# Optimization experiments

Measured on AMD Instinct MI355X. Metric: run time of the kernel, lower is better.

Reference implementation:

```python
import jax, jax.numpy as jnp
import numpy as np

N, E = 50000, 800000
IN_DIM, HID, OUT = 128, 64, 64
NEG_SLOPE = 0.2  # PyG GATConv default leaky_relu slope


def glorot(key, shape):
    fan_in, fan_out = shape[0], shape[-1]
    lim = jnp.sqrt(6.0 / (fan_in + fan_out))
    return jax.random.uniform(key, shape, minval=-lim, maxval=lim, dtype=jnp.float32)


def setup_inputs() -> dict:
    key = jax.random.key(0)
    ks = jax.random.split(key, 10)
    x = jax.random.normal(ks[0], (N, IN_DIM), dtype=jnp.float32)
    edge_index = jax.random.randint(ks[1], (2, E), 0, N, dtype=jnp.int64)
    # GATConv layer 1: heads=2, concat=False
    W1 = glorot(ks[2], (IN_DIM, 2 * HID))
    att_src1 = glorot(ks[3], (1, 2, HID))[0]   # [2, HID]
    att_dst1 = glorot(ks[4], (1, 2, HID))[0]
    b1 = jnp.zeros((HID,), jnp.float32)
    # GATConv layer 2: heads=1, concat=False
    W2 = glorot(ks[5], (HID, OUT))
    att_src2 = glorot(ks[6], (1, 1, OUT))[0]   # [1, OUT]
    att_dst2 = glorot(ks[7], (1, 1, OUT))[0]
    b2 = jnp.zeros((OUT,), jnp.float32)
    return {"x": x, "edge_index": edge_index, "W1": W1, "att_src1": att_src1,
            "att_dst1": att_dst1, "b1": b1, "W2": W2, "att_src2": att_src2,
            "att_dst2": att_dst2, "b2": b2}


def gat_conv(x, src, dst, W, att_src, att_dst, bias, heads, out_ch):
    n = x.shape[0]
    h = (x @ W).reshape(n, heads, out_ch)              # [N,H,C]
    a_src = jnp.einsum('nhc,hc->nh', h, att_src)       # [N,H]
    a_dst = jnp.einsum('nhc,hc->nh', h, att_dst)
    e = jax.nn.leaky_relu(a_src[src] + a_dst[dst], NEG_SLOPE)  # [E,H]
    # softmax over incoming edges per destination node (stable)
    e_max = jax.ops.segment_max(e, dst, num_segments=n)
    ex = jnp.exp(e - e_max[dst])
    denom = jax.ops.segment_sum(ex, dst, num_segments=n)
    alpha = ex / (denom[dst] + 1e-16)                  # [E,H]
    msg = h[src] * alpha[:, :, None]                   # [E,H,C]
    out = jax.ops.segment_sum(msg, dst, num_segments=n)
    return out.mean(axis=1) + bias                     # concat=False -> head mean


def reference(x, edge_index, W1, att_src1, att_dst1, b1, W2, att_src2, att_dst2, b2):
    n = x.shape[0]
    loop = jnp.arange(n, dtype=edge_index.dtype)
    src = jnp.concatenate([edge_index[0], loop])       # PyG add_self_loops
    dst = jnp.concatenate([edge_index[1], loop])
    x1 = gat_conv(x, src, dst, W1, att_src1, att_dst1, b1, 2, HID)
    x1 = jax.nn.elu(x1)
    # eval mode: dropedge and dropout are identity
    out = gat_conv(x1, src, dst, W2, att_src2, att_dst2, b2, 1, OUT)
    return out
```

## Files before the change

### kernel.cpp

```cpp
#include <hip/hip_runtime.h>
#include <math.h>

#define IN_DIM 128
#define HID 64
#define NEG_SLOPE 0.2f
#define CHUNK 4096
#define GCAP 6144
#define SMEM_UNION 53248
#define NBIGBLK 40

typedef __attribute__((ext_vector_type(8))) short bf16x8;
typedef __attribute__((ext_vector_type(4))) float f32x4;
typedef __attribute__((ext_vector_type(2))) float v2f;

__device__ __forceinline__ float wmax(float v){
  #pragma unroll
  for (int o = 32; o > 0; o >>= 1) v = fmaxf(v, __shfl_xor(v, o));
  return v;
}
__device__ __forceinline__ float wsum(float v){
  #pragma unroll
  for (int o = 32; o > 0; o >>= 1) v += __shfl_xor(v, o);
  return v;
}
__device__ __forceinline__ float wmax32(float v){
  #pragma unroll
  for (int o = 16; o > 0; o >>= 1) v = fmaxf(v, __shfl_xor(v, o, 32));
  return v;
}
__device__ __forceinline__ unsigned short f2bf(float f){
  union { float f; unsigned u; } v; v.f = f;
  unsigned r = v.u + 0x7fffu + ((v.u >> 16) & 1u);
  return (unsigned short)(r >> 16);
}
__device__ __forceinline__ float bl(unsigned u){
  union { unsigned u; float f; } v; v.u = u << 16; return v.f;
}
__device__ __forceinline__ float bh(unsigned u){
  union { unsigned u; float f; } v; v.u = u & 0xffff0000u; return v.f;
}
__device__ __forceinline__ v2f up2(unsigned u){
  v2f r; r[0] = bl(u); r[1] = bh(u); return r;
}

__device__ __forceinline__ void incl_scan256(int* sh, int tid){
  __shared__ int wt[4];
  int lane = tid & 63, w = tid >> 6;
  int sc = sh[tid];
  #pragma unroll
  for (int o = 1; o < 64; o <<= 1){
    int t = __shfl_up(sc, o);
    if (lane >= o) sc += t;
  }
  if (lane == 63) wt[w] = sc;
  __syncthreads();
  int add = 0;
  if (w > 0) add += wt[0];
  if (w > 1) add += wt[1];
  if (w > 2) add += wt[2];
  sh[tid] = sc + add;
  __syncthreads();
}


__device__ void scatter_body(char* smem, const unsigned* __restrict__ packed, int E,
                             const int* __restrict__ binCnt, int* __restrict__ binOff,
                             unsigned* __restrict__ binned, int bx){
  int* ib = (int*)smem;
  int* bc = ib;
  int* lh = ib + 256;
  int* lbase = ib + 512;
  int* gpos = ib + 768;
  int* lcur = ib + 1024;
  unsigned* buf = (unsigned*)(ib + 1280);
  int tid = threadIdx.x;
  int cg = binCnt[tid];
  bc[tid] = cg;
  lh[tid] = 0;
  __syncthreads();
  incl_scan256(bc, tid);
  int binBase_t = bc[tid] - cg;
  int base = bx * CHUNK;
  int rem = E - base;
  unsigned v[CHUNK / 256];
  #pragma unroll
  for (int j = 0; j < CHUNK / 256; j++){
    int i = j * 256 + tid;
    if (i < rem){ v[j] = packed[base + i]; atomicAdd(&lh[v[j] >> 24], 1); }
  }
  __syncthreads();
  lbase[tid] = lh[tid]; __syncthreads();
  incl_scan256(lbase, tid);
  int myExcl = tid ? lbase[tid - 1] : 0;
  __syncthreads();
  lbase[tid] = myExcl;
  lcur[tid] = myExcl;
  if (lh[tid] > 0) gpos[tid] = binBase_t + atomicAdd(&binOff[tid], lh[tid]);
  __syncthreads();
  #pragma unroll
  for (int j = 0; j < CHUNK / 256; j++){
    int i = j * 256 + tid;
    if (i < rem){
      int b = v[j] >> 24;
      int p = atomicAdd(&lcur[b], 1);
      buf[p] = v[j];
    }
  }
  __syncthreads();
  int cn = rem < CHUNK ? rem : CHUNK;
  for (int i = tid; i < cn; i += 256){
    unsigned u = buf[i];
    int b = u >> 24;
    binned[gpos[b] + (i - lbase[b])] = u;
  }
}

__device__ void group_body(char* smem, const unsigned* __restrict__ binned,
                           const int* __restrict__ binCnt, unsigned* __restrict__ sorted,
                           int* __restrict__ row_ptr, int N, int g){
  unsigned* A = (unsigned*)smem;
  unsigned* B = A + GCAP;
  int* ib = (int*)(B + GCAP);
  int* sc = ib;
  int* h2 = ib + 256;
  int* rs = ib + 512;
  int* cur = ib + 768;
  int tid = threadIdx.x;
  int cg = binCnt[tid];
  sc[tid] = cg;
  h2[tid] = 0;
  __syncthreads();
  incl_scan256(sc, tid);
  int base = sc[g] - binCnt[g];
  int cnt = binCnt[g]; if (cnt > GCAP) cnt = GCAP;
  __syncthreads();
  for (int i = tid; i < cnt; i += 256){
    unsigned u = binned[base + i];
    A[i] = u;
    atomicAdd(&h2[(u >> 16) & 255], 1);
  }
  __syncthreads();
  rs[tid] = h2[tid]; __syncthreads();
  incl_scan256(rs, tid);
  int excl = tid ? rs[tid - 1] : 0;
  __syncthreads();
  rs[tid] = excl; cur[tid] = excl;
  int d = g * 256 + tid;
  if (d < N) row_ptr[d] = base + excl;
  __syncthreads();
  for (int i = tid; i < cnt; i += 256){
    unsigned u = A[i];
    int p = atomicAdd(&cur[(u >> 16) & 255], 1);
    B[p] = u;
  }
  __syncthreads();
  for (int i = tid; i < cnt; i += 256)
    sorted[base + i] = B[i];
}


__device__ void gemm1_body(char* smem, const float* __restrict__ X,
                           const unsigned short* __restrict__ Wt,
                           const float* __restrict__ asrc, const float* __restrict__ adst,
                           unsigned short* __restrict__ Hb, float* __restrict__ aa,
                           int n_rows, int n0){
  const int KP = 136, CP = 132;
  unsigned short* xa = (unsigned short*)smem;
  unsigned short* wl = xa + 64 * KP;
  int tid = threadIdx.x;
  for (int idx = tid; idx < 64 * 32; idx += 256){
    int n = idx >> 5, k4 = idx & 31;
    float4 v = make_float4(0.f, 0.f, 0.f, 0.f);
    if (n0 + n < n_rows) v = *(const float4*)&X[(size_t)(n0 + n) * 128 + k4 * 4];
    ushort4 pk; pk.x = f2bf(v.x); pk.y = f2bf(v.y); pk.z = f2bf(v.z); pk.w = f2bf(v.w);
    *(ushort4*)&xa[n * KP + k4 * 4] = pk;
  }
  for (int idx = tid; idx < 128 * 16; idx += 256){
    int n = idx >> 4, k8 = idx & 15;
    uint4 v = *(const uint4*)&Wt[(size_t)n * 128 + k8 * 8];
    *(uint4*)&wl[n * KP + k8 * 8] = v;
  }
  __syncthreads();

  int lane = tid & 63, w = tid >> 6;
  int m = lane & 15, q = lane >> 4;
  f32x4 acc[4][2];
  #pragma unroll
  for (int i = 0; i < 4; i++)
    #pragma unroll
    for (int j = 0; j < 2; j++)
      #pragma unroll
      for (int r = 0; r < 4; r++) acc[i][j][r] = 0.f;
  #pragma unroll
  for (int ks = 0; ks < 4; ks++){
    bf16x8 bg[2];
    #pragma unroll
    for (int j = 0; j < 2; j++)
      bg[j] = *(const bf16x8*)&wl[((2 * w + j) * 16 + m) * KP + ks * 32 + q * 8];
    #pragma unroll
    for (int i = 0; i < 4; i++){
      bf16x8 af = *(const bf16x8*)&xa[(i * 16 + m) * KP + ks * 32 + q * 8];
      #pragma unroll
      for (int j = 0; j < 2; j++)
        acc[i][j] = __builtin_amdgcn_mfma_f32_16x16x32_bf16(af, bg[j], acc[i][j], 0, 0, 0);
    }
  }
  __syncthreads();
  float* C = (float*)smem;
  #pragma unroll
  for (int i = 0; i < 4; i++)
    #pragma unroll
    for (int j = 0; j < 2; j++)
      #pragma unroll
      for (int r = 0; r < 4; r++)
        C[(i * 16 + q * 4 + r) * CP + (2 * w + j) * 16 + m] = acc[i][j][r];
  __syncthreads();

  int row = tid >> 2;
  int c0 = (tid & 3) * 32;
  int n = n0 + row;
  int head = (tid & 3) >> 1;
  float s_p = 0.f, d_p = 0.f;
  unsigned short hb[32];
  #pragma unroll
  for (int c = 0; c < 32; c += 4){
    f32x4 v = *(const f32x4*)&C[row * CP + c0 + c];
    #pragma unroll
    for (int u = 0; u < 4; u++){
      int ch = (c0 + c + u) & 63;
      s_p += v[u] * asrc[head * 64 + ch];
      d_p += v[u] * adst[head * 64 + ch];
      hb[c + u] = f2bf(v[u]);
    }
  }
  if (n < n_rows){
    #pragma unroll
    for (int c = 0; c < 32; c += 8){
      uint4 pk;
      pk.x = (unsigned)hb[c]     | ((unsigned)hb[c + 1] << 16);
      pk.y = (unsigned)hb[c + 2] | ((unsigned)hb[c + 3] << 16);
      pk.z = (unsigned)hb[c + 4] | ((unsigned)hb[c + 5] << 16);
      pk.w = (unsigned)hb[c + 6] | ((unsigned)hb[c + 7] << 16);
      *(uint4*)&Hb[(size_t)n * 128 + c0 + c] = pk;
    }
  }
  s_p += __shfl_xor(s_p, 1);
  d_p += __shfl_xor(d_p, 1);
  if ((tid & 1) == 0 && n < n_rows){
    aa[(size_t)n * 4 + head]     = s_p;
    aa[(size_t)n * 4 + 2 + head] = d_p;
  }
}


__global__ __launch_bounds__(256) void sort_gemm_a(const unsigned* __restrict__ packed, int E,
    const int* __restrict__ binCnt, int* __restrict__ binOff, unsigned* __restrict__ binned,
    int NS, const float* __restrict__ X, const unsigned short* __restrict__ W1t,
    const float* __restrict__ asrc1, const float* __restrict__ adst1,
    unsigned short* __restrict__ h1b, float* __restrict__ aa1, int n_rows){
  __shared__ char smem[SMEM_UNION];
  int bx = blockIdx.x;
  if (bx < NS){
    scatter_body(smem, packed, E, binCnt, binOff, binned, bx);
  } else {
    gemm1_body(smem, X, W1t, asrc1, adst1, h1b, aa1, n_rows, (bx - NS) * 64);
  }
}

__global__ __launch_bounds__(256) void sort_gemm_b(const unsigned* __restrict__ binned,
    const int* __restrict__ binCnt, unsigned* __restrict__ sorted, int* __restrict__ row_ptr,
    int N, int NS, int gofs, const float* __restrict__ X, const unsigned short* __restrict__ W1t,
    const float* __restrict__ asrc1, const float* __restrict__ adst1,
    unsigned short* __restrict__ h1b, float* __restrict__ aa1, int n_rows){
  __shared__ char smem[SMEM_UNION];
  int bx = blockIdx.x;
  if (bx < NS){
    group_body(smem, binned, binCnt, sorted, row_ptr, N, bx);
  } else {
    gemm1_body(smem, X, W1t, asrc1, adst1, h1b, aa1, n_rows, (gofs + bx - NS) * 64);
  }
}


__global__ __launch_bounds__(256) void prep(const int* __restrict__ ei, int E, int NBLK,
                                            unsigned* __restrict__ packed,
                                            int* __restrict__ binCnt,
                                            const float* __restrict__ W1,
                                            const float* __restrict__ W2,
                                            unsigned short* __restrict__ W1t,
                                            unsigned short* __restrict__ W2t,
                                            int* __restrict__ row_ptr, int N){
  int tid = threadIdx.x;
  if ((int)blockIdx.x < NBLK){
    __shared__ int lh[256];
    lh[tid] = 0; __syncthreads();
    int base = blockIdx.x * CHUNK;
    if (((E & 3) == 0) && (base + CHUNK <= E)){
      #pragma unroll
      for (int j = 0; j < 4; j++){
        int e0 = base + j * 1024 + tid * 4;
        int4 sv = *(const int4*)&ei[e0];
        int4 dv = *(const int4*)&ei[E + e0];
        uint4 pk;
        pk.x = ((unsigned)dv.x << 16) | (unsigned)sv.x;
        pk.y = ((unsigned)dv.y << 16) | (unsigned)sv.y;
        pk.z = ((unsigned)dv.z << 16) | (unsigned)sv.z;
        pk.w = ((unsigned)dv.w << 16) | (unsigned)sv.w;
        *(uint4*)&packed[e0] = pk;
        atomicAdd(&lh[dv.x >> 8], 1);
        atomicAdd(&lh[dv.y >> 8], 1);
        atomicAdd(&lh[dv.z >> 8], 1);
        atomicAdd(&lh[dv.w >> 8], 1);
      }
    } else {
      #pragma unroll
      for (int j = 0; j < CHUNK / 256; j++){
        int e = base + j * 256 + tid;
        if (e < E){
          unsigned s = (unsigned)ei[e];
          unsigned d = (unsigned)ei[E + e];
          packed[e] = (d << 16) | s;
          atomicAdd(&lh[d >> 8], 1);
        }
      }
    }
    __syncthreads();
    if (lh[tid] > 0) atomicAdd(&binCnt[tid], lh[tid]);
  } else {
    int t = (blockIdx.x - NBLK) * 256 + tid;
    if (t < 128 * 128){
      int n = t >> 7, k = t & 127;
      W1t[n * 128 + k] = f2bf(W1[k * 128 + n]);
    }
    int t2 = t - 128 * 128;
    if (t2 >= 0 && t2 < 64 * 64){
      int n = t2 >> 6, k = t2 & 63;
      W2t[n * 64 + k] = f2bf(W2[k * 64 + n]);
    }
    if (t == 0) row_ptr[N] = E;
  }
}


__global__ __launch_bounds__(512) void gemm2_mfma(const unsigned short* __restrict__ Xb,
    const unsigned short* __restrict__ Wt, const float* __restrict__ asrc,
    const float* __restrict__ adst, unsigned short* __restrict__ Hb,
    float* __restrict__ aa, int n_rows)
{
  constexpr int K = 64, NC = 64;
  constexpr int MT = 128;
  constexpr int KP = K + 8;
  constexpr int CP = NC + 4;
  constexpr int MFW = 4;
  constexpr unsigned SM1 = (unsigned)(MT + NC) * KP * 2;
  constexpr unsigned SM2 = (unsigned)MT * CP * 4;
  __shared__ char smem[SM1 > SM2 ? SM1 : SM2];
  unsigned short* xa = (unsigned short*)smem;
  unsigned short* wl = xa + MT * KP;
  int tid = threadIdx.x;
  int n0 = blockIdx.x * MT;

  for (int idx = tid; idx < MT * (K / 8); idx += 512){
    int n = idx >> 3, k8 = idx & 7;
    uint4 v = make_uint4(0u, 0u, 0u, 0u);
    if (n0 + n < n_rows) v = *(const uint4*)&Xb[(size_t)(n0 + n) * K + k8 * 8];
    *(uint4*)&xa[n * KP + k8 * 8] = v;
  }
  for (int idx = tid; idx < NC * (K / 8); idx += 512){
    int n = idx >> 3, k8 = idx & 7;
    uint4 v = *(const uint4*)&Wt[(size_t)n * K + k8 * 8];
    *(uint4*)&wl[n * KP + k8 * 8] = v;
  }
  __syncthreads();

  int lane = tid & 63, w = tid >> 6;
  int m = lane & 15, q = lane >> 4;
  int nf = w & 3;
  int mseg = w >> 2;
  f32x4 acc[MFW];
  #pragma unroll
  for (int i = 0; i < MFW; i++)
    #pragma unroll
    for (int r = 0; r < 4; r++) acc[i][r] = 0.f;

  #pragma unroll
  for (int ks = 0; ks < K / 32; ks++){
    bf16x8 bg = *(const bf16x8*)&wl[(nf * 16 + m) * KP + ks * 32 + q * 8];
    #pragma unroll
    for (int i = 0; i < MFW; i++){
      bf16x8 af = *(const bf16x8*)&xa[((mseg * MFW + i) * 16 + m) * KP + ks * 32 + q * 8];
      acc[i] = __builtin_amdgcn_mfma_f32_16x16x32_bf16(af, bg, acc[i], 0, 0, 0);
    }
  }
  __syncthreads();
  float* C = (float*)smem;
  #pragma unroll
  for (int i = 0; i < MFW; i++)
    #pragma unroll
    for (int r = 0; r < 4; r++)
      C[((mseg * MFW + i) * 16 + q * 4 + r) * CP + nf * 16 + m] = acc[i][r];
  __syncthreads();

  constexpr int CH = NC / 4;
  int row = tid >> 2;
  int c0 = (tid & 3) * CH;
  int n = n0 + row;
  float s_p = 0.f, d_p = 0.f;
  unsigned short hb[CH];
  #pragma unroll
  for (int c = 0; c < CH; c += 4){
    f32x4 v = *(const f32x4*)&C[row * CP + c0 + c];
    #pragma unroll
    for (int u = 0; u < 4; u++){
      int ch = (c0 + c + u) & 63;
      s_p += v[u] * asrc[ch];
      d_p += v[u] * adst[ch];
      hb[c + u] = f2bf(v[u]);
    }
  }
  if (n < n_rows){
    #pragma unroll
    for (int c = 0; c < CH; c += 8){
      uint4 pk;
      pk.x = (unsigned)hb[c]     | ((unsigned)hb[c + 1] << 16);
      pk.y = (unsigned)hb[c + 2] | ((unsigned)hb[c + 3] << 16);
      pk.z = (unsigned)hb[c + 4] | ((unsigned)hb[c + 5] << 16);
      pk.w = (unsigned)hb[c + 6] | ((unsigned)hb[c + 7] << 16);
      *(uint4*)&Hb[(size_t)n * NC + c0 + c] = pk;
    }
  }
  s_p += __shfl_xor(s_p, 1);
  d_p += __shfl_xor(d_p, 1);
  s_p += __shfl_xor(s_p, 2);
  d_p += __shfl_xor(d_p, 2);
  if ((tid & 3) == 0 && n < n_rows){
    aa[(size_t)n * 2]     = s_p;
    aa[(size_t)n * 2 + 1] = d_p;
  }
}


__device__ void agg1_one64(int d, int lane, const int* __restrict__ row_ptr,
                           const unsigned* __restrict__ sorted, const float* __restrict__ aa,
                           const unsigned short* __restrict__ h1b, const float* __restrict__ b1,
                           unsigned short* __restrict__ x1b){
  int rp0 = row_ptr[d];
  int deg = row_ptr[d + 1] - rp0;
  float2 adv = *(const float2*)&aa[d * 4 + 2];
  int s = -1;
  if (lane < deg) s = (int)(sorted[rp0 + lane] & 0xffffu);
  else if (lane == deg) s = d;
  float e0 = -INFINITY, e1 = -INFINITY;
  if (s >= 0){
    float2 asv = *(const float2*)&aa[s * 4];
    float t0 = asv.x + adv.x;
    float t1 = asv.y + adv.y;
    e0 = t0 >= 0.f ? t0 : NEG_SLOPE * t0;
    e1 = t1 >= 0.f ? t1 : NEG_SLOPE * t1;
  }
  float m0 = wmax(e0), m1 = wmax(e1);
  float p0 = (s >= 0) ? __expf(e0 - m0) : 0.f;
  float p1 = (s >= 0) ? __expf(e1 - m1) : 0.f;
  float al0 = p0 * __builtin_amdgcn_rcpf(wsum(p0) + 1e-16f);
  float al1 = p1 * __builtin_amdgcn_rcpf(wsum(p1) + 1e-16f);
  int ne = deg + 1;
  int g = lane >> 4, c = lane & 15;
  bool hsel = (c < 8);
  const uint4* hp = (const uint4*)h1b;
  v2f acc[4] = {{0.f,0.f},{0.f,0.f},{0.f,0.f},{0.f,0.f}};
  for (int j0 = 0; j0 < ne; j0 += 16){
    uint4 v[4]; float av[4];
    #pragma unroll
    for (int b = 0; b < 4; b++){
      int j = j0 + b * 4 + g;
      int sj = __shfl(s, j);
      float a0 = __shfl(al0, j);
      float a1 = __shfl(al1, j);
      av[b] = hsel ? a0 : a1;
      if (j < ne) v[b] = hp[(size_t)sj * 16 + c];
    }
    #pragma unroll
    for (int b = 0; b < 4; b++){
      if (j0 + b * 4 + g < ne){
        v2f aw = {av[b], av[b]};
        acc[0] = aw * up2(v[b].x) + acc[0];
        acc[1] = aw * up2(v[b].y) + acc[1];
        acc[2] = aw * up2(v[b].z) + acc[2];
        acc[3] = aw * up2(v[b].w) + acc[3];
      }
    }
  }
  float accf[8] = {acc[0][0], acc[0][1], acc[1][0], acc[1][1],
                   acc[2][0], acc[2][1], acc[3][0], acc[3][1]};
  #pragma unroll
  for (int i = 0; i < 8; i++){
    accf[i] += __shfl_xor(accf[i], 16);
    accf[i] += __shfl_xor(accf[i], 32);
  }
  float outv[8];
  #pragma unroll
  for (int i = 0; i < 8; i++){
    float o = __shfl_xor(accf[i], 8);
    outv[i] = 0.5f * (accf[i] + o);
  }
  if (g == 0 && c < 8){
    unsigned short hb[8];
    #pragma unroll
    for (int i = 0; i < 8; i++){
      float v = outv[i] + b1[c * 8 + i];
      float r = v > 0.f ? v : __expf(v) - 1.0f;
      hb[i] = f2bf(r);
    }
    uint4 pk;
    pk.x = (unsigned)hb[0] | ((unsigned)hb[1] << 16);
    pk.y = (unsigned)hb[2] | ((unsigned)hb[3] << 16);
    pk.z = (unsigned)hb[4] | ((unsigned)hb[5] << 16);
    pk.w = (unsigned)hb[6] | ((unsigned)hb[7] << 16);
    *(uint4*)&x1b[(size_t)d * 64 + c * 8] = pk;
  }
}

__global__ __launch_bounds__(512) void agg_layer1(const int* __restrict__ row_ptr,
    const unsigned* __restrict__ sorted, const float* __restrict__ aa,
    const unsigned short* __restrict__ h1b, const float* __restrict__ b1,
    unsigned short* __restrict__ x1b, int n_nodes, int npair, int nsweep){
  int tid = threadIdx.x;
  int lane = tid & 63;
  if ((int)blockIdx.x >= npair){
    int sw = (blockIdx.x - npair) * 8 + (tid >> 6);
    int chunk = (n_nodes + nsweep - 1) / nsweep;
    int a = sw * chunk;
    int bnd = a + chunk; if (bnd > n_nodes) bnd = n_nodes;
    for (int i0 = a; i0 < bnd; i0 += 64){
      int idx = i0 + lane;
      int dg = 0;
      if (idx < bnd) dg = row_ptr[idx + 1] - row_ptr[idx];
      unsigned long long m = __ballot(dg > 31);
      while (m){
        int bit = __ffsll((long long)m) - 1;
        m &= m - 1;
        agg1_one64(i0 + bit, lane, row_ptr, sorted, aa, h1b, b1, x1b);
      }
    }
    return;
  }
  int wid = (blockIdx.x << 3) + (tid >> 6);
  int half = lane >> 5, l32 = lane & 31;
  int d = wid * 2 + half;
  if (wid * 2 >= n_nodes) return;
  bool valid = d < n_nodes;
  int rp0 = 0, deg = -1;
  if (valid){ rp0 = row_ptr[d]; deg = row_ptr[d + 1] - rp0; }
  bool ok = valid && deg <= 31;
  int ne = ok ? deg + 1 : 0;
  int s = -1;
  if (ok){
    if (l32 < deg) s = (int)(sorted[rp0 + l32] & 0xffffu);
    else if (l32 == deg) s = d;
  }
  float2 adv = make_float2(0.f, 0.f);
  if (valid) adv = *(const float2*)&aa[d * 4 + 2];
  float e0 = -INFINITY, e1 = -INFINITY;
  if (s >= 0){
    float2 asv = *(const float2*)&aa[s * 4];
    float t0 = asv.x + adv.x;
    float t1 = asv.y + adv.y;
    e0 = t0 >= 0.f ? t0 : NEG_SLOPE * t0;
    e1 = t1 >= 0.f ? t1 : NEG_SLOPE * t1;
  }
  float m0 = wmax32(e0), m1 = wmax32(e1);
  float p0 = (s >= 0) ? __expf(e0 - m0) : 0.f;
  float p1 = (s >= 0) ? __expf(e1 - m1) : 0.f;
  int g = l32 >> 4, c = l32 & 15;
  bool hsel = (c < 8);
  const uint4* hp = (const uint4*)h1b;
  v2f acc[4] = {{0.f,0.f},{0.f,0.f},{0.f,0.f},{0.f,0.f}};
  float dn = 0.f;
  {
    int sj[8]; float pv[8];
    #pragma unroll
    for (int b = 0; b < 8; b++){
      int j = 2 * b + g;
      sj[b] = __shfl(s, j, 32);
      float q0 = __shfl(p0, j, 32);
      float q1 = __shfl(p1, j, 32);
      pv[b] = hsel ? q0 : q1;
    }
    uint4 v[8];
    #pragma unroll
    for (int b = 0; b < 8; b++){
      if (2 * b + g < ne) v[b] = hp[(size_t)sj[b] * 16 + c];
    }
    #pragma unroll
    for (int b = 0; b < 8; b++){
      if (2 * b + g < ne){
        v2f aw = {pv[b], pv[b]};
        acc[0] = aw * up2(v[b].x) + acc[0];
        acc[1] = aw * up2(v[b].y) + acc[1];
        acc[2] = aw * up2(v[b].z) + acc[2];
        acc[3] = aw * up2(v[b].w) + acc[3];
        dn += pv[b];
      }
    }
  }
  if (ne > 16){
    int sj[8]; float pv[8];
    #pragma unroll
    for (int b = 0; b < 8; b++){
      int j = 16 + 2 * b + g;
      sj[b] = __shfl(s, j, 32);
      float q0 = __shfl(p0, j, 32);
      float q1 = __shfl(p1, j, 32);
      pv[b] = hsel ? q0 : q1;
    }
    uint4 v[8];
    #pragma unroll
    for (int b = 0; b < 8; b++){
      if (16 + 2 * b + g < ne) v[b] = hp[(size_t)sj[b] * 16 + c];
    }
    #pragma unroll
    for (int b = 0; b < 8; b++){
      if (16 + 2 * b + g < ne){
        v2f aw = {pv[b], pv[b]};
        acc[0] = aw * up2(v[b].x) + acc[0];
        acc[1] = aw * up2(v[b].y) + acc[1];
        acc[2] = aw * up2(v[b].z) + acc[2];
        acc[3] = aw * up2(v[b].w) + acc[3];
        dn += pv[b];
      }
    }
  }
  float accf[8] = {acc[0][0], acc[0][1], acc[1][0], acc[1][1],
                   acc[2][0], acc[2][1], acc[3][0], acc[3][1]};
  #pragma unroll
  for (int i = 0; i < 8; i++) accf[i] += __shfl_xor(accf[i], 16, 32);
  dn += __shfl_xor(dn, 16, 32);
  float inv = __builtin_amdgcn_rcpf(dn);
  float outv[8];
  #pragma unroll
  for (int i = 0; i < 8; i++){
    float r = accf[i] * inv;
    float o = __shfl_xor(r, 8, 32);
    outv[i] = 0.5f * (r + o);
  }
  if (ok && l32 < 8){
    unsigned short hb[8];
    #pragma unroll
    for (int i = 0; i < 8; i++){
      float v = outv[i] + b1[l32 * 8 + i];
      float r = v > 0.f ? v : __expf(v) - 1.0f;
      hb[i] = f2bf(r);
    }
    uint4 pk;
    pk.x = (unsigned)hb[0] | ((unsigned)hb[1] << 16);
    pk.y = (unsigned)hb[2] | ((unsigned)hb[3] << 16);
    pk.z = (unsigned)hb[4] | ((unsigned)hb[5] << 16);
    pk.w = (unsigned)hb[6] | ((unsigned)hb[7] << 16);
    *(uint4*)&x1b[(size_t)d * 64 + l32 * 8] = pk;
  }
}

__device__ void agg2_one64(int d, int lane, const int* __restrict__ row_ptr,
                           const unsigned* __restrict__ sorted, const float* __restrict__ aa,
                           const unsigned short* __restrict__ h2b, const float* __restrict__ b2,
                           float* __restrict__ out){
  int rp0 = row_ptr[d];
  int deg = row_ptr[d + 1] - rp0;
  float ad = aa[d * 2 + 1];
  int s = -1;
  if (lane < deg) s = (int)(sorted[rp0 + lane] & 0xffffu);
  else if (lane == deg) s = d;
  float e = -INFINITY;
  if (s >= 0){
    float t = aa[s * 2 + 0] + ad;
    e = t >= 0.f ? t : NEG_SLOPE * t;
  }
  float m = wmax(e);
  float p = (s >= 0) ? __expf(e - m) : 0.f;
  float al = p * __builtin_amdgcn_rcpf(wsum(p) + 1e-16f);
  int ne = deg + 1;
  int g = lane >> 3, c = lane & 7;
  const uint4* hp = (const uint4*)h2b;
  v2f acc[4] = {{0.f,0.f},{0.f,0.f},{0.f,0.f},{0.f,0.f}};
  for (int j0 = 0; j0 < ne; j0 += 32){
    uint4 v[4]; float av[4];
    #pragma unroll
    for (int b = 0; b < 4; b++){
      int j = j0 + b * 8 + g;
      int sj = __shfl(s, j);
      av[b] = __shfl(al, j);
      if (j < ne) v[b] = hp[(size_t)sj * 8 + c];
    }
    #pragma unroll
    for (int b = 0; b < 4; b++){
      if (j0 + b * 8 + g < ne){
        v2f aw = {av[b], av[b]};
        acc[0] = aw * up2(v[b].x) + acc[0];
        acc[1] = aw * up2(v[b].y) + acc[1];
        acc[2] = aw * up2(v[b].z) + acc[2];
        acc[3] = aw * up2(v[b].w) + acc[3];
      }
    }
  }
  float accf[8] = {acc[0][0], acc[0][1], acc[1][0], acc[1][1],
                   acc[2][0], acc[2][1], acc[3][0], acc[3][1]};
  #pragma unroll
  for (int i = 0; i < 8; i++){
    accf[i] += __shfl_xor(accf[i], 8);
    accf[i] += __shfl_xor(accf[i], 16);
    accf[i] += __shfl_xor(accf[i], 32);
  }
  if (lane < 8){
    float r[8];
    #pragma unroll
    for (int i = 0; i < 8; i++) r[i] = accf[i] + b2[lane * 8 + i];
    float* q = &out[(size_t)d * 64 + lane * 8];
    *(float4*)q       = make_float4(r[0], r[1], r[2], r[3]);
    *(float4*)(q + 4) = make_float4(r[4], r[5], r[6], r[7]);
  }
}

__global__ __launch_bounds__(512) void agg_layer2(const int* __restrict__ row_ptr,
    const unsigned* __restrict__ sorted, const float* __restrict__ aa,
    const unsigned short* __restrict__ h2b, const float* __restrict__ b2,
    float* __restrict__ out, int n_nodes, int npair, int nsweep){
  int tid = threadIdx.x;
  int lane = tid & 63;
  if ((int)blockIdx.x >= npair){
    int sw = (blockIdx.x - npair) * 8 + (tid >> 6);
    int chunk = (n_nodes + nsweep - 1) / nsweep;
    int a = sw * chunk;
    int bnd = a + chunk; if (bnd > n_nodes) bnd = n_nodes;
    for (int i0 = a; i0 < bnd; i0 += 64){
      int idx = i0 + lane;
      int dg = 0;
      if (idx < bnd) dg = row_ptr[idx + 1] - row_ptr[idx];
      unsigned long long m = __ballot(dg > 31);
      while (m){
        int bit = __ffsll((long long)m) - 1;
        m &= m - 1;
        agg2_one64(i0 + bit, lane, row_ptr, sorted, aa, h2b, b2, out);
      }
    }
    return;
  }
  int wid = (blockIdx.x << 3) + (tid >> 6);
  int half = lane >> 5, l32 = lane & 31;
  int d = wid * 2 + half;
  if (wid * 2 >= n_nodes) return;
  bool valid = d < n_nodes;
  int rp0 = 0, deg = -1;
  if (valid){ rp0 = row_ptr[d]; deg = row_ptr[d + 1] - rp0; }
  bool ok = valid && deg <= 31;
  int ne = ok ? deg + 1 : 0;
  int s = -1;
  if (ok){
    if (l32 < deg) s = (int)(sorted[rp0 + l32] & 0xffffu);
    else if (l32 == deg) s = d;
  }
  float ad = valid ? aa[d * 2 + 1] : 0.f;
  float e = -INFINITY;
  if (s >= 0){
    float t = aa[s * 2 + 0] + ad;
    e = t >= 0.f ? t : NEG_SLOPE * t;
  }
  float m = wmax32(e);
  float p = (s >= 0) ? __expf(e - m) : 0.f;
  int g = l32 >> 3, c = l32 & 7;
  const uint4* hp = (const uint4*)h2b;
  v2f acc[4] = {{0.f,0.f},{0.f,0.f},{0.f,0.f},{0.f,0.f}};
  float dn = 0.f;
  {
    int sj[8]; float pv[8];
    #pragma unroll
    for (int b = 0; b < 8; b++){
      int j = 4 * b + g;
      sj[b] = __shfl(s, j, 32);
      pv[b] = __shfl(p, j, 32);
    }
    uint4 v[8];
    #pragma unroll
    for (int b = 0; b < 8; b++){
      if (4 * b + g < ne) v[b] = hp[(size_t)sj[b] * 8 + c];
    }
    #pragma unroll
    for (int b = 0; b < 8; b++){
      if (4 * b + g < ne){
        v2f aw = {pv[b], pv[b]};
        acc[0] = aw * up2(v[b].x) + acc[0];
        acc[1] = aw * up2(v[b].y) + acc[1];
        acc[2] = aw * up2(v[b].z) + acc[2];
        acc[3] = aw * up2(v[b].w) + acc[3];
        dn += pv[b];
      }
    }
  }
  float accf[8] = {acc[0][0], acc[0][1], acc[1][0], acc[1][1],
                   acc[2][0], acc[2][1], acc[3][0], acc[3][1]};
  #pragma unroll
  for (int i = 0; i < 8; i++){
    accf[i] += __shfl_xor(accf[i], 8, 32);
    accf[i] += __shfl_xor(accf[i], 16, 32);
  }
  dn += __shfl_xor(dn, 8, 32);
  dn += __shfl_xor(dn, 16, 32);
  float inv = __builtin_amdgcn_rcpf(dn);
  if (ok && l32 < 8){
    float r[8];
    #pragma unroll
    for (int i = 0; i < 8; i++) r[i] = accf[i] * inv + b2[l32 * 8 + i];
    float* q = &out[(size_t)d * 64 + l32 * 8];
    *(float4*)q       = make_float4(r[0], r[1], r[2], r[3]);
    *(float4*)(q + 4) = make_float4(r[4], r[5], r[6], r[7]);
  }
}

extern "C" void kernel_launch(void* const* d_in, const int* in_sizes, int n_in,
                              void* d_out, int out_size, void* d_ws, size_t ws_size,
                              hipStream_t stream){
  const float* x     = (const float*)d_in[0];
  const int*   ei    = (const int*)d_in[1];
  const float* W1    = (const float*)d_in[2];
  const float* asrc1 = (const float*)d_in[3];
  const float* adst1 = (const float*)d_in[4];
  const float* b1    = (const float*)d_in[5];
  const float* W2    = (const float*)d_in[6];
  const float* asrc2 = (const float*)d_in[7];
  const float* adst2 = (const float*)d_in[8];
  const float* b2    = (const float*)d_in[9];
  float* out = (float*)d_out;
  int N = in_sizes[0] / IN_DIM;
  int E = in_sizes[1] / 2;
  int NG = (N + 255) >> 8;
  int NBLK = (E + CHUNK - 1) / CHUNK;
  int npair = (N + 15) / 16;
  int GT = (N + 63) / 64;
  int GA = GT / 2;
  int GB = GT - GA;

  char* p = (char*)d_ws;
  unsigned short* h1b = (unsigned short*)p;  p += (size_t)N * 128 * 2;
  unsigned short* h2b = (unsigned short*)p;  p += (size_t)N * 64 * 2;
  unsigned short* x1b = (unsigned short*)p;  p += (size_t)N * 64 * 2;
  float* aa1 = (float*)p;                    p += (size_t)N * 4 * 4;
  float* aa2 = (float*)p;                    p += (size_t)N * 2 * 4;
  unsigned* packed = (unsigned*)p;           p += (size_t)E * 4;
  unsigned* binned = (unsigned*)p;           p += (size_t)E * 4;
  unsigned* sorted = (unsigned*)p;           p += (size_t)E * 4;
  int* row_ptr   = (int*)p;                  p += (size_t)(N + 1) * 4;
  int* binCnt    = (int*)p;                  p += 256 * 4;
  int* binOff    = (int*)p;                  p += 256 * 4;
  unsigned short* W1t = (unsigned short*)p;  p += 128 * 128 * 2;
  unsigned short* W2t = (unsigned short*)p;

  hipMemsetAsync(binCnt, 0, 512 * sizeof(int), stream);
  prep<<<NBLK + 80, 256, 0, stream>>>(ei, E, NBLK, packed, binCnt,
                                      W1, W2, W1t, W2t, row_ptr, N);
  sort_gemm_a<<<NBLK + GA, 256, 0, stream>>>(packed, E, binCnt, binOff, binned,
                                             NBLK, x, W1t, asrc1, adst1, h1b, aa1, N);
  sort_gemm_b<<<NG + GB, 256, 0, stream>>>(binned, binCnt, sorted, row_ptr, N,
                                           NG, GA, x, W1t, asrc1, adst1, h1b, aa1, N);
  agg_layer1<<<npair + NBIGBLK, 512, 0, stream>>>(row_ptr, sorted, aa1, h1b, b1, x1b,
                                                  N, npair, NBIGBLK * 8);
  gemm2_mfma<<<(N + 127) / 128, 512, 0, stream>>>(x1b, W2t, asrc2, adst2, h2b, aa2, N);
  agg_layer2<<<npair + NBIGBLK, 512, 0, stream>>>(row_ptr, sorted, aa2, h2b, b2, out,
                                                  N, npair, NBIGBLK * 8);
}
```

Measured before the change: 208.6 us.

## Reorder layer-2 GEMM after aggregation and fold attention vectors into layer-1 epilogue

Precomputes W2·att_src2 and W2·att_dst2 in prep so the layer-2 attention logits are computed directly from x1 inside the layer-1 aggregation epilogue. Layer 2 then aggregates x1 (same width) first and applies W2 plus bias afterwards in a final GEMM, which removes the separate h2 materialisation pass. It also drops the packed edge buffer: the scatter reads edge_index directly and prep only builds the histogram. The cost is an extra bf16 rounding of the aggregated features before the final GEMM, and a changed order of summation.

```diff
diff --git a/kernel.cpp b/kernel.cpp
--- a/kernel.cpp
+++ b/kernel.cpp
@@ -63,7 +63,7 @@
 }
 
 
-__device__ void scatter_body(char* smem, const unsigned* __restrict__ packed, int E,
+__device__ void scatter_body(char* smem, const int* __restrict__ ei, int E,
                              const int* __restrict__ binCnt, int* __restrict__ binOff,
                              unsigned* __restrict__ binned, int bx){
   int* ib = (int*)smem;
@@ -83,27 +83,64 @@
   int base = bx * CHUNK;
   int rem = E - base;
   unsigned v[CHUNK / 256];
-  #pragma unroll
-  for (int j = 0; j < CHUNK / 256; j++){
-    int i = j * 256 + tid;
-    if (i < rem){ v[j] = packed[base + i]; atomicAdd(&lh[v[j] >> 24], 1); }
-  }
-  __syncthreads();
-  lbase[tid] = lh[tid]; __syncthreads();
-  incl_scan256(lbase, tid);
-  int myExcl = tid ? lbase[tid - 1] : 0;
-  __syncthreads();
-  lbase[tid] = myExcl;
-  lcur[tid] = myExcl;
-  if (lh[tid] > 0) gpos[tid] = binBase_t + atomicAdd(&binOff[tid], lh[tid]);
-  __syncthreads();
-  #pragma unroll
-  for (int j = 0; j < CHUNK / 256; j++){
-    int i = j * 256 + tid;
-    if (i < rem){
+  if (((E & 3) == 0) && (base + CHUNK <= E)){
+    #pragma unroll
+    for (int j = 0; j < 4; j++){
+      int e0 = base + j * 1024 + tid * 4;
+      int4 sv = *(const int4*)&ei[e0];
+      int4 dv = *(const int4*)&ei[E + e0];
+      v[j * 4 + 0] = ((unsigned)dv.x << 16) | (unsigned)sv.x;
+      v[j * 4 + 1] = ((unsigned)dv.y << 16) | (unsigned)sv.y;
+      v[j * 4 + 2] = ((unsigned)dv.z << 16) | (unsigned)sv.z;
+      v[j * 4 + 3] = ((unsigned)dv.w << 16) | (unsigned)sv.w;
+      atomicAdd(&lh[dv.x >> 8], 1);
+      atomicAdd(&lh[dv.y >> 8], 1);
+      atomicAdd(&lh[dv.z >> 8], 1);
+      atomicAdd(&lh[dv.w >> 8], 1);
+    }
+    __syncthreads();
+    lbase[tid] = lh[tid]; __syncthreads();
+    incl_scan256(lbase, tid);
+    int myExcl = tid ? lbase[tid - 1] : 0;
+    __syncthreads();
+    lbase[tid] = myExcl;
+    lcur[tid] = myExcl;
+    if (lh[tid] > 0) gpos[tid] = binBase_t + atomicAdd(&binOff[tid], lh[tid]);
+    __syncthreads();
+    #pragma unroll
+    for (int j = 0; j < CHUNK / 256; j++){
       int b = v[j] >> 24;
       int p = atomicAdd(&lcur[b], 1);
       buf[p] = v[j];
+    }
+  } else {
+    #pragma unroll
+    for (int j = 0; j < CHUNK / 256; j++){
+      int i = j * 256 + tid;
+      if (i < rem){
+        unsigned s = (unsigned)ei[base + i];
+        unsigned d = (unsigned)ei[E + base + i];
+        v[j] = (d << 16) | s;
+        atomicAdd(&lh[v[j] >> 24], 1);
+      }
+    }
+    __syncthreads();
+    lbase[tid] = lh[tid]; __syncthreads();
+    incl_scan256(lbase, tid);
+    int myExcl = tid ? lbase[tid - 1] : 0;
+    __syncthreads();
+    lbase[tid] = myExcl;
+    lcur[tid] = myExcl;
+    if (lh[tid] > 0) gpos[tid] = binBase_t + atomicAdd(&binOff[tid], lh[tid]);
+    __syncthreads();
+    #pragma unroll
+    for (int j = 0; j < CHUNK / 256; j++){
+      int i = j * 256 + tid;
+      if (i < rem){
+        int b = v[j] >> 24;
+        int p = atomicAdd(&lcur[b], 1);
+        buf[p] = v[j];
+      }
     }
   }
   __syncthreads();
@@ -253,7 +290,7 @@
 }
 
 
-__global__ __launch_bounds__(256) void sort_gemm_a(const unsigned* __restrict__ packed, int E,
+__global__ __launch_bounds__(256) void sort_gemm_a(const int* __restrict__ ei, int E,
     const int* __restrict__ binCnt, int* __restrict__ binOff, unsigned* __restrict__ binned,
     int NS, const float* __restrict__ X, const unsigned short* __restrict__ W1t,
     const float* __restrict__ asrc1, const float* __restrict__ adst1,
@@ -261,7 +298,7 @@
   __shared__ char smem[SMEM_UNION];
   int bx = blockIdx.x;
   if (bx < NS){
-    scatter_body(smem, packed, E, binCnt, binOff, binned, bx);
+    scatter_body(smem, ei, E, binCnt, binOff, binned, bx);
   } else {
     gemm1_body(smem, X, W1t, asrc1, adst1, h1b, aa1, n_rows, (bx - NS) * 64);
   }
@@ -283,12 +320,15 @@
 
 
 __global__ __launch_bounds__(256) void prep(const int* __restrict__ ei, int E, int NBLK,
-                                            unsigned* __restrict__ packed,
                                             int* __restrict__ binCnt,
                                             const float* __restrict__ W1,
                                             const float* __restrict__ W2,
+                                            const float* __restrict__ asrc2,
+                                            const float* __restrict__ adst2,
                                             unsigned short* __restrict__ W1t,
                                             unsigned short* __restrict__ W2t,
+                                            float* __restrict__ w2a,
+                                            float* __restrict__ w2b,
                                             int* __restrict__ row_ptr, int N){
   int tid = threadIdx.x;
   if ((int)blockIdx.x < NBLK){
@@ -299,14 +339,7 @@
       #pragma unroll
       for (int j = 0; j < 4; j++){
         int e0 = base + j * 1024 + tid * 4;
-        int4 sv = *(const int4*)&ei[e0];
         int4 dv = *(const int4*)&ei[E + e0];
-        uint4 pk;
-        pk.x = ((unsigned)dv.x << 16) | (unsigned)sv.x;
-        pk.y = ((unsigned)dv.y << 16) | (unsigned)sv.y;
-        pk.z = ((unsigned)dv.z << 16) | (unsigned)sv.z;
-        pk.w = ((unsigned)dv.w << 16) | (unsigned)sv.w;
-        *(uint4*)&packed[e0] = pk;
         atomicAdd(&lh[dv.x >> 8], 1);
         atomicAdd(&lh[dv.y >> 8], 1);
         atomicAdd(&lh[dv.z >> 8], 1);
@@ -316,12 +349,7 @@
       #pragma unroll
       for (int j = 0; j < CHUNK / 256; j++){
         int e = base + j * 256 + tid;
-        if (e < E){
-          unsigned s = (unsigned)ei[e];
-          unsigned d = (unsigned)ei[E + e];
-          packed[e] = (d << 16) | s;
-          atomicAdd(&lh[d >> 8], 1);
-        }
+        if (e < E) atomicAdd(&lh[ei[E + e] >> 8], 1);
       }
     }
     __syncthreads();
@@ -337,15 +365,26 @@
       int n = t2 >> 6, k = t2 & 63;
       W2t[n * 64 + k] = f2bf(W2[k * 64 + n]);
     }
+    int t3 = t - (128 * 128 + 64 * 64);
+    if (t3 >= 0 && t3 < 64){
+      float sa = 0.f, sb = 0.f;
+      #pragma unroll
+      for (int n = 0; n < 64; n++){
+        float wv = W2[t3 * 64 + n];
+        sa += wv * asrc2[n];
+        sb += wv * adst2[n];
+      }
+      w2a[t3] = sa;
+      w2b[t3] = sb;
+    }
     if (t == 0) row_ptr[N] = E;
   }
 }
 
 
-__global__ __launch_bounds__(512) void gemm2_mfma(const unsigned short* __restrict__ Xb,
-    const unsigned short* __restrict__ Wt, const float* __restrict__ asrc,
-    const float* __restrict__ adst, unsigned short* __restrict__ Hb,
-    float* __restrict__ aa, int n_rows)
+__global__ __launch_bounds__(512) void gemm_out(const unsigned short* __restrict__ Xb,
+    const unsigned short* __restrict__ Wt, const float* __restrict__ b2,
+    float* __restrict__ out, int n_rows)
 {
   constexpr int K = 64, NC = 64;
   constexpr int MT = 128;
@@ -401,41 +440,20 @@
       C[((mseg * MFW + i) * 16 + q * 4 + r) * CP + nf * 16 + m] = acc[i][r];
   __syncthreads();
 
-  constexpr int CH = NC / 4;
   int row = tid >> 2;
-  int c0 = (tid & 3) * CH;
+  int c0 = (tid & 3) * 16;
   int n = n0 + row;
-  float s_p = 0.f, d_p = 0.f;
-  unsigned short hb[CH];
-  #pragma unroll
-  for (int c = 0; c < CH; c += 4){
-    f32x4 v = *(const f32x4*)&C[row * CP + c0 + c];
-    #pragma unroll
-    for (int u = 0; u < 4; u++){
-      int ch = (c0 + c + u) & 63;
-      s_p += v[u] * asrc[ch];
-      d_p += v[u] * adst[ch];
-      hb[c + u] = f2bf(v[u]);
-    }
-  }
   if (n < n_rows){
     #pragma unroll
-    for (int c = 0; c < CH; c += 8){
-      uint4 pk;
-      pk.x = (unsigned)hb[c]     | ((unsigned)hb[c + 1] << 16);
-      pk.y = (unsigned)hb[c + 2] | ((unsigned)hb[c + 3] << 16);
-      pk.z = (unsigned)hb[c + 4] | ((unsigned)hb[c + 5] << 16);
-      pk.w = (unsigned)hb[c + 6] | ((unsigned)hb[c + 7] << 16);
-      *(uint4*)&Hb[(size_t)n * NC + c0 + c] = pk;
-    }
-  }
-  s_p += __shfl_xor(s_p, 1);
-  d_p += __shfl_xor(d_p, 1);
-  s_p += __shfl_xor(s_p, 2);
-  d_p += __shfl_xor(d_p, 2);
-  if ((tid & 3) == 0 && n < n_rows){
-    aa[(size_t)n * 2]     = s_p;
-    aa[(size_t)n * 2 + 1] = d_p;
+    for (int c = 0; c < 16; c += 4){
+      f32x4 v = *(const f32x4*)&C[row * CP + c0 + c];
+      float4 o;
+      o.x = v[0] + b2[c0 + c];
+      o.y = v[1] + b2[c0 + c + 1];
+      o.z = v[2] + b2[c0 + c + 2];
+      o.w = v[3] + b2[c0 + c + 3];
+      *(float4*)&out[(size_t)n * 64 + c0 + c] = o;
+    }
   }
 }
 
@@ -443,7 +461,8 @@
 __device__ void agg1_one64(int d, int lane, const int* __restrict__ row_ptr,
                            const unsigned* __restrict__ sorted, const float* __restrict__ aa,
                            const unsigned short* __restrict__ h1b, const float* __restrict__ b1,
-                           unsigned short* __restrict__ x1b){
+                           const float* __restrict__ w2a, const float* __restrict__ w2b,
+                           unsigned short* __restrict__ x1b, float* __restrict__ aa2){
   int rp0 = row_ptr[d];
   int deg = row_ptr[d + 1] - rp0;
   float2 adv = *(const float2*)&aa[d * 4 + 2];
@@ -505,11 +524,12 @@
   }
   if (g == 0 && c < 8){
     unsigned short hb[8];
+    float rr[8];
     #pragma unroll
     for (int i = 0; i < 8; i++){
       float v = outv[i] + b1[c * 8 + i];
-      float r = v > 0.f ? v : __expf(v) - 1.0f;
-      hb[i] = f2bf(r);
+      rr[i] = v > 0.f ? v : __expf(v) - 1.0f;
+      hb[i] = f2bf(rr[i]);
     }
     uint4 pk;
     pk.x = (unsigned)hb[0] | ((unsigned)hb[1] << 16);
@@ -517,13 +537,28 @@
     pk.z = (unsigned)hb[4] | ((unsigned)hb[5] << 16);
     pk.w = (unsigned)hb[6] | ((unsigned)hb[7] << 16);
     *(uint4*)&x1b[(size_t)d * 64 + c * 8] = pk;
+    float sd = 0.f, dd = 0.f;
+    #pragma unroll
+    for (int i = 0; i < 8; i++){
+      sd += rr[i] * w2a[c * 8 + i];
+      dd += rr[i] * w2b[c * 8 + i];
+    }
+    sd += __shfl_xor(sd, 1); dd += __shfl_xor(dd, 1);
+    sd += __shfl_xor(sd, 2); dd += __shfl_xor(dd, 2);
+    sd += __shfl_xor(sd, 4); dd += __shfl_xor(dd, 4);
+    if (c == 0){
+      aa2[(size_t)d * 2]     = sd;
+      aa2[(size_t)d * 2 + 1] = dd;
+    }
   }
 }
 
 __global__ __launch_bounds__(512) void agg_layer1(const int* __restrict__ row_ptr,
     const unsigned* __restrict__ sorted, const float* __restrict__ aa,
     const unsigned short* __restrict__ h1b, const float* __restrict__ b1,
-    unsigned short* __restrict__ x1b, int n_nodes, int npair, int nsweep){
+    const float* __restrict__ w2a, const float* __restrict__ w2b,
+    unsigned short* __restrict__ x1b, float* __restrict__ aa2,
+    int n_nodes, int npair, int nsweep){
   int tid = threadIdx.x;
   int lane = tid & 63;
   if ((int)blockIdx.x >= npair){
@@ -539,7 +574,7 @@
       while (m){
         int bit = __ffsll((long long)m) - 1;
         m &= m - 1;
-        agg1_one64(i0 + bit, lane, row_ptr, sorted, aa, h1b, b1, x1b);
+        agg1_one64(i0 + bit, lane, row_ptr, sorted, aa, h1b, b1, w2a, w2b, x1b, aa2);
       }
     }
     return;
@@ -645,11 +680,12 @@
   }
   if (ok && l32 < 8){
     unsigned short hb[8];
+    float rr[8];
     #pragma unroll
     for (int i = 0; i < 8; i++){
       float v = outv[i] + b1[l32 * 8 + i];
-      float r = v > 0.f ? v : __expf(v) - 1.0f;
-      hb[i] = f2bf(r);
+      rr[i] = v > 0.f ? v : __expf(v) - 1.0f;
+      hb[i] = f2bf(rr[i]);
     }
     uint4 pk;
     pk.x = (unsigned)hb[0] | ((unsigned)hb[1] << 16);
@@ -657,13 +693,26 @@
     pk.z = (unsigned)hb[4] | ((unsigned)hb[5] << 16);
     pk.w = (unsigned)hb[6] | ((unsigned)hb[7] << 16);
     *(uint4*)&x1b[(size_t)d * 64 + l32 * 8] = pk;
+    float sd = 0.f, dd = 0.f;
+    #pragma unroll
+    for (int i = 0; i < 8; i++){
+      sd += rr[i] * w2a[l32 * 8 + i];
+      dd += rr[i] * w2b[l32 * 8 + i];
+    }
+    sd += __shfl_xor(sd, 1, 32); dd += __shfl_xor(dd, 1, 32);
+    sd += __shfl_xor(sd, 2, 32); dd += __shfl_xor(dd, 2, 32);
+    sd += __shfl_xor(sd, 4, 32); dd += __shfl_xor(dd, 4, 32);
+    if (l32 == 0){
+      aa2[(size_t)d * 2]     = sd;
+      aa2[(size_t)d * 2 + 1] = dd;
+    }
   }
 }
 
 __device__ void agg2_one64(int d, int lane, const int* __restrict__ row_ptr,
                            const unsigned* __restrict__ sorted, const float* __restrict__ aa,
-                           const unsigned short* __restrict__ h2b, const float* __restrict__ b2,
-                           float* __restrict__ out){
+                           const unsigned short* __restrict__ xb,
+                           unsigned short* __restrict__ y1b){
   int rp0 = row_ptr[d];
   int deg = row_ptr[d + 1] - rp0;
   float ad = aa[d * 2 + 1];
@@ -680,7 +729,7 @@
   float al = p * __builtin_amdgcn_rcpf(wsum(p) + 1e-16f);
   int ne = deg + 1;
   int g = lane >> 3, c = lane & 7;
-  const uint4* hp = (const uint4*)h2b;
+  const uint4* hp = (const uint4*)xb;
   v2f acc[4] = {{0.f,0.f},{0.f,0.f},{0.f,0.f},{0.f,0.f}};
   for (int j0 = 0; j0 < ne; j0 += 32){
     uint4 v[4]; float av[4];
@@ -711,19 +760,22 @@
     accf[i] += __shfl_xor(accf[i], 32);
   }
   if (lane < 8){
-    float r[8];
-    #pragma unroll
-    for (int i = 0; i < 8; i++) r[i] = accf[i] + b2[lane * 8 + i];
-    float* q = &out[(size_t)d * 64 + lane * 8];
-    *(float4*)q       = make_float4(r[0], r[1], r[2], r[3]);
-    *(float4*)(q + 4) = make_float4(r[4], r[5], r[6], r[7]);
+    unsigned short hb[8];
+    #pragma unroll
+    for (int i = 0; i < 8; i++) hb[i] = f2bf(accf[i]);
+    uint4 pk;
+    pk.x = (unsigned)hb[0] | ((unsigned)hb[1] << 16);
+    pk.y = (unsigned)hb[2] | ((unsigned)hb[3] << 16);
+    pk.z = (unsigned)hb[4] | ((unsigned)hb[5] << 16);
+    pk.w = (unsigned)hb[6] | ((unsigned)hb[7] << 16);
+    *(uint4*)&y1b[(size_t)d * 64 + lane * 8] = pk;
   }
 }
 
 __global__ __launch_bounds__(512) void agg_layer2(const int* __restrict__ row_ptr,
     const unsigned* __restrict__ sorted, const float* __restrict__ aa,
-    const unsigned short* __restrict__ h2b, const float* __restrict__ b2,
-    float* __restrict__ out, int n_nodes, int npair, int nsweep){
+    const unsigned short* __restrict__ xb, unsigned short* __restrict__ y1b,
+    int n_nodes, int npair, int nsweep){
   int tid = threadIdx.x;
   int lane = tid & 63;
   if ((int)blockIdx.x >= npair){
@@ -739,7 +791,7 @@
       while (m){
         int bit = __ffsll((long long)m) - 1;
         m &= m - 1;
-        agg2_one64(i0 + bit, lane, row_ptr, sorted, aa, h2b, b2, out);
+        agg2_one64(i0 + bit, lane, row_ptr, sorted, aa, xb, y1b);
       }
     }
     return;
@@ -767,7 +819,7 @@
   float m = wmax32(e);
   float p = (s >= 0) ? __expf(e - m) : 0.f;
   int g = l32 >> 3, c = l32 & 7;
-  const uint4* hp = (const uint4*)h2b;
+  const uint4* hp = (const uint4*)xb;
   v2f acc[4] = {{0.f,0.f},{0.f,0.f},{0.f,0.f},{0.f,0.f}};
   float dn = 0.f;
   {
@@ -806,12 +858,15 @@
   dn += __shfl_xor(dn, 16, 32);
   float inv = __builtin_amdgcn_rcpf(dn);
   if (ok && l32 < 8){
-    float r[8];
-    #pragma unroll
-    for (int i = 0; i < 8; i++) r[i] = accf[i] * inv + b2[l32 * 8 + i];
-    float* q = &out[(size_t)d * 64 + l32 * 8];
-    *(float4*)q       = make_float4(r[0], r[1], r[2], r[3]);
-    *(float4*)(q + 4) = make_float4(r[4], r[5], r[6], r[7]);
+    unsigned short hb[8];
+    #pragma unroll
+    for (int i = 0; i < 8; i++) hb[i] = f2bf(accf[i] * inv);
+    uint4 pk;
+    pk.x = (unsigned)hb[0] | ((unsigned)hb[1] << 16);
+    pk.y = (unsigned)hb[2] | ((unsigned)hb[3] << 16);
+    pk.z = (unsigned)hb[4] | ((unsigned)hb[5] << 16);
+    pk.w = (unsigned)hb[6] | ((unsigned)hb[7] << 16);
+    *(uint4*)&y1b[(size_t)d * 64 + l32 * 8] = pk;
   }
 }
 
@@ -840,29 +895,31 @@
 
   char* p = (char*)d_ws;
   unsigned short* h1b = (unsigned short*)p;  p += (size_t)N * 128 * 2;
-  unsigned short* h2b = (unsigned short*)p;  p += (size_t)N * 64 * 2;
   unsigned short* x1b = (unsigned short*)p;  p += (size_t)N * 64 * 2;
+  unsigned short* y1b = (unsigned short*)p;  p += (size_t)N * 64 * 2;
   float* aa1 = (float*)p;                    p += (size_t)N * 4 * 4;
   float* aa2 = (float*)p;                    p += (size_t)N * 2 * 4;
-  unsigned* packed = (unsigned*)p;           p += (size_t)E * 4;
   unsigned* binned = (unsigned*)p;           p += (size_t)E * 4;
   unsigned* sorted = (unsigned*)p;           p += (size_t)E * 4;
   int* row_ptr   = (int*)p;                  p += (size_t)(N + 1) * 4;
   int* binCnt    = (int*)p;                  p += 256 * 4;
   int* binOff    = (int*)p;                  p += 256 * 4;
   unsigned short* W1t = (unsigned short*)p;  p += 128 * 128 * 2;
-  unsigned short* W2t = (unsigned short*)p;
+  unsigned short* W2t = (unsigned short*)p;  p += 64 * 64 * 2;
+  float* w2a = (float*)p;                    p += 64 * 4;
+  float* w2b = (float*)p;
 
   hipMemsetAsync(binCnt, 0, 512 * sizeof(int), stream);
-  prep<<<NBLK + 80, 256, 0, stream>>>(ei, E, NBLK, packed, binCnt,
-                                      W1, W2, W1t, W2t, row_ptr, N);
-  sort_gemm_a<<<NBLK + GA, 256, 0, stream>>>(packed, E, binCnt, binOff, binned,
+  prep<<<NBLK + 81, 256, 0, stream>>>(ei, E, NBLK, binCnt, W1, W2, asrc2, adst2,
+                                      W1t, W2t, w2a, w2b, row_ptr, N);
+  sort_gemm_a<<<NBLK + GA, 256, 0, stream>>>(ei, E, binCnt, binOff, binned,
                                              NBLK, x, W1t, asrc1, adst1, h1b, aa1, N);
   sort_gemm_b<<<NG + GB, 256, 0, stream>>>(binned, binCnt, sorted, row_ptr, N,
                                            NG, GA, x, W1t, asrc1, adst1, h1b, aa1, N);
-  agg_layer1<<<npair + NBIGBLK, 512, 0, stream>>>(row_ptr, sorted, aa1, h1b, b1, x1b,
+  agg_layer1<<<npair + NBIGBLK, 512, 0, stream>>>(row_ptr, sorted, aa1, h1b, b1,
+                                                  w2a, w2b, x1b, aa2,
                                                   N, npair, NBIGBLK * 8);
-  gemm2_mfma<<<(N + 127) / 128, 512, 0, stream>>>(x1b, W2t, asrc2, adst2, h2b, aa2, N);
-  agg_layer2<<<npair + NBIGBLK, 512, 0, stream>>>(row_ptr, sorted, aa2, h2b, b2, out,
+  agg_layer2<<<npair + NBIGBLK, 512, 0, stream>>>(row_ptr, sorted, aa2, x1b, y1b,
                                                   N, npair, NBIGBLK * 8);
-}
+  gemm_out<<<(N + 127) / 128, 512, 0, stream>>>(y1b, W2t, b2, out, N);
+}
```

New measurement: 208.3 us. Within noise of the previous version (-0.2%).
